# Kernel optimization log

Measured on AMD Instinct MI355X. Metric: run time of the kernel, lower is better.

The kernel has to match this reference:

```python
import jax, jax.numpy as jnp
import numpy as np

B, G = 32, 8          # batch, num_genres
N, T = 64, 64         # notes_size, timestep_size (input)
D, O = 32, 32         # notes_out, timestep_out (output)


def setup_inputs() -> dict:
    key = jax.random.key(0)
    k1, k2, k3, k4, k5 = jax.random.split(key, 5)
    x = jax.random.normal(k1, (B, N, T), dtype=jnp.float32)
    y = jax.random.uniform(k2, (B, G), dtype=jnp.float32)
    weight = jax.random.normal(k3, (G, D, O, N, T), dtype=jnp.float32) * 0.02
    bias = jax.random.normal(k4, (D * O,), dtype=jnp.float32) * 0.02
    mask = jax.random.randint(k5, (O, T), 0, 2).astype(jnp.float32)
    return {"x": x, "y": y, "weight": weight, "bias": bias, "mask": mask}


def reference(x, y, weight, bias, mask):
    # Fused form of:
    #   mw  = einsum('gdont,ot->gdont', weight, mask)
    #   mw2 = einsum('gdont,bg->bdont', mw, y)      # huge intermediate avoided
    #   out = einsum('bnt,bdont->bdo', x, mw2) + bias
    mw = weight * mask[None, None, :, None, :]          # (g,d,o,n,t)
    xw = jnp.einsum('bnt,gdont->bgdo', x, mw)           # contract n,t first
    out = jnp.einsum('bg,bgdo->bdo', y, xw)             # (b,d,o)
    return out + bias.reshape(D, O)[None, :, :]
```

## Files before the change

kernel.cpp:

```cpp
#include <hip/hip_runtime.h>
#include <hip/hip_bf16.h>

typedef __bf16 bf16x8 __attribute__((ext_vector_type(8)));
typedef float f32x4 __attribute__((ext_vector_type(4)));

#define G 8
#define B 32
#define D 32
#define O 32
#define K 4096
#define T 64
#define KSPLIT 2
#define KCHUNK (K / KSPLIT)
#define BK 256
#define NSTEP (KCHUNK / BK)
#define MROWS 16

#define XB_ELEMS (B * K)

__global__ __launch_bounds__(256) void prep_and_init(const float* __restrict__ x,
                                                     const float* __restrict__ bias,
                                                     __bf16* __restrict__ xb,
                                                     float* __restrict__ out) {
    int tid = blockIdx.x * 256 + threadIdx.x;
    if (tid < 16384) {
        int b = (tid >> 2) & 31;
        int k = (tid >> 7) * 32 + (tid & 3) * 8;
        const float4 x0 = *(const float4*)(x + b * K + k);
        const float4 x1 = *(const float4*)(x + b * K + k + 4);
        bf16x8 r;
        r[0] = (__bf16)x0.x; r[1] = (__bf16)x0.y; r[2] = (__bf16)x0.z; r[3] = (__bf16)x0.w;
        r[4] = (__bf16)x1.x; r[5] = (__bf16)x1.y; r[6] = (__bf16)x1.z; r[7] = (__bf16)x1.w;
        *(bf16x8*)(xb + (size_t)tid * 8) = r;
    } else {
        int t2 = tid - 16384;
        out[t2] = bias[t2 & 1023];
    }
}

__global__ __launch_bounds__(128) void gemm_main(const float* __restrict__ W,
                                                 const __bf16* __restrict__ xb,
                                                 const float* __restrict__ mask,
                                                 const float* __restrict__ y,
                                                 float* __restrict__ out) {
    __shared__ float ldsW[2][MROWS * BK];
    const int d = blockIdx.x, g = blockIdx.y;
    const int oh = blockIdx.z & 1, ks = blockIdx.z >> 1;
    const int wid  = threadIdx.x >> 6;
    const int lane = threadIdx.x & 63;
    const int bh = wid;
    const int l15 = lane & 15, g16 = lane >> 4;

    const int lds_ro = l15 * 1024 + ((g16 * 32) ^ ((l15 & 7) * 16));

    const float* mrow = mask + (oh * 16 + l15) * T + g16 * 8;
    const float4 me0 = *(const float4*)(mrow);
    const float4 me1 = *(const float4*)(mrow + 4);
    const float4 mo0 = *(const float4*)(mrow + 32);
    const float4 mo1 = *(const float4*)(mrow + 36);

    const __bf16* xbl = xb + (size_t)(ks * (KCHUNK / 32)) * 1024
                           + (bh * 16 + l15) * 32 + g16 * 8;

    const size_t wrow0 = ((size_t)(g * D + d) * O + oh * 16 + 8 * wid) * K
                         + (size_t)ks * KCHUNK;

    f32x4 acc = {0.f, 0.f, 0.f, 0.f};

#define STAGE(buf, step)                                                          \
    {                                                                             \
        _Pragma("unroll")                                                         \
        for (int i = 0; i < 8; ++i) {                                             \
            const int row = 8 * wid + i;                                          \
            const char* src = (const char*)(W + wrow0 + (size_t)i * K             \
                                            + (size_t)(step) * BK)                \
                              + ((lane * 16) ^ (i * 16));                         \
            __builtin_amdgcn_global_load_lds(                                     \
                (const __attribute__((address_space(1))) void*)src,               \
                (__attribute__((address_space(3))) void*)((char*)&ldsW[buf][0]    \
                                                          + row * 1024),          \
                16, 0,  2);                                             \
        }                                                                         \
    }

    STAGE(0, 0);
    __syncthreads();

    int cur = 0;
    for (int step = 0; step < NSTEP; ++step) {
        if (step + 1 < NSTEP) STAGE(cur ^ 1, step + 1);

        const char* lb = (const char*)&ldsW[cur][0];
        const __bf16* xs = xbl + (size_t)(step * 8) * 1024;
        #pragma unroll
        for (int s = 0; s < 8; ++s) {
            const int a0 = lds_ro + s * 128;
            const f32x4 alo = *(const f32x4*)(lb + a0);
            const f32x4 ahi = *(const f32x4*)(lb + (a0 ^ 16));
            const float4 ms0 = (s & 1) ? mo0 : me0;
            const float4 ms1 = (s & 1) ? mo1 : me1;
            bf16x8 af;
            af[0] = (__bf16)(alo[0] * ms0.x); af[1] = (__bf16)(alo[1] * ms0.y);
            af[2] = (__bf16)(alo[2] * ms0.z); af[3] = (__bf16)(alo[3] * ms0.w);
            af[4] = (__bf16)(ahi[0] * ms1.x); af[5] = (__bf16)(ahi[1] * ms1.y);
            af[6] = (__bf16)(ahi[2] * ms1.z); af[7] = (__bf16)(ahi[3] * ms1.w);
            const bf16x8 bfr = *(const bf16x8*)(xs + (size_t)s * 1024);
            acc = __builtin_amdgcn_mfma_f32_16x16x32_bf16(af, bfr, acc, 0, 0, 0);
        }
        __syncthreads();
        cur ^= 1;
    }
#undef STAGE

    const int bg = bh * 16 + l15;
    const float yv = y[bg * G + g];
    float* op = out + bg * (D * O) + d * O + oh * 16;
    #pragma unroll
    for (int i = 0; i < 4; ++i)
        unsafeAtomicAdd(op + g16 * 4 + i, yv * acc[i]);
}

extern "C" void kernel_launch(void* const* d_in, const int* in_sizes, int n_in,
                              void* d_out, int out_size, void* d_ws, size_t ws_size,
                              hipStream_t stream) {
    const float* x    = (const float*)d_in[0];
    const float* y    = (const float*)d_in[1];
    const float* w    = (const float*)d_in[2];
    const float* bias = (const float*)d_in[3];
    const float* mask = (const float*)d_in[4];
    float* out = (float*)d_out;

    __bf16* xbp = (__bf16*)d_ws;

    prep_and_init<<<192, 256, 0, stream>>>(x, bias, xbp, out);
    gemm_main<<<dim3(D, G, 4), 128, 0, stream>>>(w, xbp, mask, y, out);
}
```

Measured before the change: 37.60 us.

## Replace LDS-direct loads with register-staged triple-buffered prefetch pipeline

Weight tiles are now loaded with ordinary global loads into a three-deep register ring, prefetched three steps ahead, and written to double-buffered LDS after each compute step. The K loop is fully unrolled with scheduling barriers and explicit lgkmcnt waits plus raw s_barrier in place of __syncthreads. The goal is more memory-level parallelism, so the weight stream's global latency is hidden behind the MFMA work. The cost is higher register pressure from 24 f32x4 prefetch registers (launch bounds now request 2 blocks) and explicit LDS stores in place of direct-to-LDS loads.

```diff
diff --git a/kernel.cpp b/kernel.cpp
--- a/kernel.cpp
+++ b/kernel.cpp
@@ -38,11 +38,11 @@
     }
 }
 
-__global__ __launch_bounds__(128) void gemm_main(const float* __restrict__ W,
-                                                 const __bf16* __restrict__ xb,
-                                                 const float* __restrict__ mask,
-                                                 const float* __restrict__ y,
-                                                 float* __restrict__ out) {
+__global__ __launch_bounds__(128, 2) void gemm_main(const float* __restrict__ W,
+                                                    const __bf16* __restrict__ xb,
+                                                    const float* __restrict__ mask,
+                                                    const float* __restrict__ y,
+                                                    float* __restrict__ out) {
     __shared__ float ldsW[2][MROWS * BK];
     const int d = blockIdx.x, g = blockIdx.y;
     const int oh = blockIdx.z & 1, ks = blockIdx.z >> 1;
@@ -66,51 +66,76 @@
                          + (size_t)ks * KCHUNK;
 
     f32x4 acc = {0.f, 0.f, 0.f, 0.f};
+    f32x4 rg[3][8];
 
-#define STAGE(buf, step)                                                          \
+#define RELOAD(sA, stepn)                                                         \
+    {                                                                             \
+        _Pragma("unroll")                                                         \
+        for (int i = 0; i < 8; ++i)                                               \
+            rg[sA][i] = *(const f32x4*)(W + wrow0 + (size_t)i * K                 \
+                                        + (stepn) * BK + lane * 4);               \
+    }
+#define DSWRITE(buf, sB)                                                          \
     {                                                                             \
         _Pragma("unroll")                                                         \
         for (int i = 0; i < 8; ++i) {                                             \
             const int row = 8 * wid + i;                                          \
-            const char* src = (const char*)(W + wrow0 + (size_t)i * K             \
-                                            + (size_t)(step) * BK)                \
-                              + ((lane * 16) ^ (i * 16));                         \
-            __builtin_amdgcn_global_load_lds(                                     \
-                (const __attribute__((address_space(1))) void*)src,               \
-                (__attribute__((address_space(3))) void*)((char*)&ldsW[buf][0]    \
-                                                          + row * 1024),          \
-                16, 0,  2);                                             \
+            *(f32x4*)((char*)&ldsW[buf][0] + row * 1024                           \
+                      + ((lane * 16) ^ (i * 16))) = rg[sB][i];                    \
+        }                                                                         \
+    }
+#define COMPUTE(t)                                                                \
+    {                                                                             \
+        const char* lb = (const char*)&ldsW[(t) & 1][0];                          \
+        const __bf16* xs = xbl + (size_t)((t) * 8) * 1024;                        \
+        _Pragma("unroll")                                                         \
+        for (int s = 0; s < 8; ++s) {                                             \
+            const int a0 = lds_ro + s * 128;                                      \
+            const f32x4 alo = *(const f32x4*)(lb + a0);                           \
+            const f32x4 ahi = *(const f32x4*)(lb + (a0 ^ 16));                    \
+            const float4 ms0 = (s & 1) ? mo0 : me0;                               \
+            const float4 ms1 = (s & 1) ? mo1 : me1;                               \
+            bf16x8 af;                                                            \
+            af[0] = (__bf16)(alo[0] * ms0.x); af[1] = (__bf16)(alo[1] * ms0.y);   \
+            af[2] = (__bf16)(alo[2] * ms0.z); af[3] = (__bf16)(alo[3] * ms0.w);   \
+            af[4] = (__bf16)(ahi[0] * ms1.x); af[5] = (__bf16)(ahi[1] * ms1.y);   \
+            af[6] = (__bf16)(ahi[2] * ms1.z); af[7] = (__bf16)(ahi[3] * ms1.w);   \
+            const bf16x8 bfr = *(const bf16x8*)(xs + (size_t)s * 1024);           \
+            acc = __builtin_amdgcn_mfma_f32_16x16x32_bf16(af, bfr, acc, 0, 0, 0); \
+        }                                                                         \
+    }
+#define STEP(t, sA, sB)                                                           \
+    {                                                                             \
+        if ((t) + 3 < NSTEP) RELOAD(sA, (t) + 3);                                 \
+        __builtin_amdgcn_sched_barrier(0);                                        \
+        COMPUTE(t);                                                               \
+        __builtin_amdgcn_sched_barrier(0);                                        \
+        if ((t) + 1 < NSTEP) {                                                    \
+            DSWRITE(((t) + 1) & 1, sB);                                           \
+            asm volatile("s_waitcnt lgkmcnt(0)" ::: "memory");                    \
+            __builtin_amdgcn_s_barrier();                                         \
         }                                                                         \
     }
 
-    STAGE(0, 0);
-    __syncthreads();
+    RELOAD(0, 0);
+    RELOAD(1, 1);
+    RELOAD(2, 2);
+    DSWRITE(0, 0);
+    asm volatile("s_waitcnt lgkmcnt(0)" ::: "memory");
+    __builtin_amdgcn_s_barrier();
 
-    int cur = 0;
-    for (int step = 0; step < NSTEP; ++step) {
-        if (step + 1 < NSTEP) STAGE(cur ^ 1, step + 1);
-
-        const char* lb = (const char*)&ldsW[cur][0];
-        const __bf16* xs = xbl + (size_t)(step * 8) * 1024;
-        #pragma unroll
-        for (int s = 0; s < 8; ++s) {
-            const int a0 = lds_ro + s * 128;
-            const f32x4 alo = *(const f32x4*)(lb + a0);
-            const f32x4 ahi = *(const f32x4*)(lb + (a0 ^ 16));
-            const float4 ms0 = (s & 1) ? mo0 : me0;
-            const float4 ms1 = (s & 1) ? mo1 : me1;
-            bf16x8 af;
-            af[0] = (__bf16)(alo[0] * ms0.x); af[1] = (__bf16)(alo[1] * ms0.y);
-            af[2] = (__bf16)(alo[2] * ms0.z); af[3] = (__bf16)(alo[3] * ms0.w);
-            af[4] = (__bf16)(ahi[0] * ms1.x); af[5] = (__bf16)(ahi[1] * ms1.y);
-            af[6] = (__bf16)(ahi[2] * ms1.z); af[7] = (__bf16)(ahi[3] * ms1.w);
-            const bf16x8 bfr = *(const bf16x8*)(xs + (size_t)s * 1024);
-            acc = __builtin_amdgcn_mfma_f32_16x16x32_bf16(af, bfr, acc, 0, 0, 0);
-        }
-        __syncthreads();
-        cur ^= 1;
-    }
-#undef STAGE
+    STEP(0, 0, 1)
+    STEP(1, 1, 2)
+    STEP(2, 2, 0)
+    STEP(3, 0, 1)
+    STEP(4, 1, 2)
+    STEP(5, 2, 0)
+    STEP(6, 0, 1)
+    STEP(7, 1, 2)
+#undef RELOAD
+#undef DSWRITE
+#undef COMPUTE
+#undef STEP
 
     const int bg = bh * 16 + l15;
     const float yv = y[bg * G + g];
```

After: 43.73 us. +16.3%, slower.

## Replace LDS staging with direct register loads, single-wave blocks, deeper K-split

Applied to the files above, without the earlier changes.

Drops the LDS double-buffer built with global_load_lds and has each single-wave block load its weight rows straight into registers, using a three-deep software pipeline of loads ahead of the MFMAs. Each wave now covers both batch halves with two accumulators, so each masked weight fragment is converted once and feeds two MFMAs. K-split goes from 2 to 8, giving 4096 small blocks to raise memory-level parallelism on the weight stream. The cost is four times more atomic adds into the output and uncoalesced per-lane row reads of the weights.

```diff
diff --git a/kernel.cpp b/kernel.cpp
--- a/kernel.cpp
+++ b/kernel.cpp
@@ -10,11 +10,9 @@
 #define O 32
 #define K 4096
 #define T 64
-#define KSPLIT 2
-#define KCHUNK (K / KSPLIT)
-#define BK 256
-#define NSTEP (KCHUNK / BK)
-#define MROWS 16
+#define KSPLIT 8
+#define KCH (K / KSPLIT)
+#define NKT (KCH / 32)
 
 #define XB_ELEMS (B * K)
 
@@ -38,20 +36,15 @@
     }
 }
 
-__global__ __launch_bounds__(128) void gemm_main(const float* __restrict__ W,
-                                                 const __bf16* __restrict__ xb,
-                                                 const float* __restrict__ mask,
-                                                 const float* __restrict__ y,
-                                                 float* __restrict__ out) {
-    __shared__ float ldsW[2][MROWS * BK];
+__global__ __launch_bounds__(64, 4) void gemm_main(const float* __restrict__ W,
+                                                   const __bf16* __restrict__ xb,
+                                                   const float* __restrict__ mask,
+                                                   const float* __restrict__ y,
+                                                   float* __restrict__ out) {
     const int d = blockIdx.x, g = blockIdx.y;
     const int oh = blockIdx.z & 1, ks = blockIdx.z >> 1;
-    const int wid  = threadIdx.x >> 6;
-    const int lane = threadIdx.x & 63;
-    const int bh = wid;
+    const int lane = threadIdx.x;
     const int l15 = lane & 15, g16 = lane >> 4;
-
-    const int lds_ro = l15 * 1024 + ((g16 * 32) ^ ((l15 & 7) * 16));
 
     const float* mrow = mask + (oh * 16 + l15) * T + g16 * 8;
     const float4 me0 = *(const float4*)(mrow);
@@ -59,65 +52,67 @@
     const float4 mo0 = *(const float4*)(mrow + 32);
     const float4 mo1 = *(const float4*)(mrow + 36);
 
-    const __bf16* xbl = xb + (size_t)(ks * (KCHUNK / 32)) * 1024
-                           + (bh * 16 + l15) * 32 + g16 * 8;
+    const float* wl = W + ((size_t)(g * D + d) * O + oh * 16 + l15) * K
+                        + ks * KCH + g16 * 8;
+    const __bf16* xL = xb + (size_t)(ks * NKT) * 1024 + l15 * 32 + g16 * 8;
+    const __bf16* xH = xL + 512;
 
-    const size_t wrow0 = ((size_t)(g * D + d) * O + oh * 16 + 8 * wid) * K
-                         + (size_t)ks * KCHUNK;
+    f32x4 accL = {0.f, 0.f, 0.f, 0.f};
+    f32x4 accH = {0.f, 0.f, 0.f, 0.f};
 
-    f32x4 acc = {0.f, 0.f, 0.f, 0.f};
+    f32x4 w0_0, w1_0, w0_1, w1_1, w0_2, w1_2;
+    bf16x8 xl_0, xh_0, xl_1, xh_1, xl_2, xh_2;
 
-#define STAGE(buf, step)                                                          \
+#define LOADSET(p, ktl)                                                           \
     {                                                                             \
-        _Pragma("unroll")                                                         \
-        for (int i = 0; i < 8; ++i) {                                             \
-            const int row = 8 * wid + i;                                          \
-            const char* src = (const char*)(W + wrow0 + (size_t)i * K             \
-                                            + (size_t)(step) * BK)                \
-                              + ((lane * 16) ^ (i * 16));                         \
-            __builtin_amdgcn_global_load_lds(                                     \
-                (const __attribute__((address_space(1))) void*)src,               \
-                (__attribute__((address_space(3))) void*)((char*)&ldsW[buf][0]    \
-                                                          + row * 1024),          \
-                16, 0,  2);                                             \
-        }                                                                         \
+        w0_##p = *(const f32x4*)(wl + (ktl) * 32);                                \
+        w1_##p = *(const f32x4*)(wl + (ktl) * 32 + 4);                            \
+        xl_##p = *(const bf16x8*)(xL + (size_t)(ktl) * 1024);                     \
+        xh_##p = *(const bf16x8*)(xH + (size_t)(ktl) * 1024);                     \
+    }
+#define COMP(p, ktl)                                                              \
+    {                                                                             \
+        const float4 ms0 = ((ktl) & 1) ? mo0 : me0;                               \
+        const float4 ms1 = ((ktl) & 1) ? mo1 : me1;                               \
+        bf16x8 af;                                                                \
+        af[0] = (__bf16)(w0_##p[0] * ms0.x); af[1] = (__bf16)(w0_##p[1] * ms0.y); \
+        af[2] = (__bf16)(w0_##p[2] * ms0.z); af[3] = (__bf16)(w0_##p[3] * ms0.w); \
+        af[4] = (__bf16)(w1_##p[0] * ms1.x); af[5] = (__bf16)(w1_##p[1] * ms1.y); \
+        af[6] = (__bf16)(w1_##p[2] * ms1.z); af[7] = (__bf16)(w1_##p[3] * ms1.w); \
+        accL = __builtin_amdgcn_mfma_f32_16x16x32_bf16(af, xl_##p, accL, 0, 0, 0);\
+        accH = __builtin_amdgcn_mfma_f32_16x16x32_bf16(af, xh_##p, accH, 0, 0, 0);\
     }
 
-    STAGE(0, 0);
-    __syncthreads();
+    LOADSET(0, 0)
+    LOADSET(1, 1)
+    LOADSET(2, 2)  COMP(0, 0)
+    LOADSET(0, 3)  COMP(1, 1)
+    LOADSET(1, 4)  COMP(2, 2)
+    LOADSET(2, 5)  COMP(0, 3)
+    LOADSET(0, 6)  COMP(1, 4)
+    LOADSET(1, 7)  COMP(2, 5)
+    LOADSET(2, 8)  COMP(0, 6)
+    LOADSET(0, 9)  COMP(1, 7)
+    LOADSET(1, 10) COMP(2, 8)
+    LOADSET(2, 11) COMP(0, 9)
+    LOADSET(0, 12) COMP(1, 10)
+    LOADSET(1, 13) COMP(2, 11)
+    LOADSET(2, 14) COMP(0, 12)
+    LOADSET(0, 15) COMP(1, 13)
+    COMP(2, 14)
+    COMP(0, 15)
+#undef LOADSET
+#undef COMP
 
-    int cur = 0;
-    for (int step = 0; step < NSTEP; ++step) {
-        if (step + 1 < NSTEP) STAGE(cur ^ 1, step + 1);
-
-        const char* lb = (const char*)&ldsW[cur][0];
-        const __bf16* xs = xbl + (size_t)(step * 8) * 1024;
-        #pragma unroll
-        for (int s = 0; s < 8; ++s) {
-            const int a0 = lds_ro + s * 128;
-            const f32x4 alo = *(const f32x4*)(lb + a0);
-            const f32x4 ahi = *(const f32x4*)(lb + (a0 ^ 16));
-            const float4 ms0 = (s & 1) ? mo0 : me0;
-            const float4 ms1 = (s & 1) ? mo1 : me1;
-            bf16x8 af;
-            af[0] = (__bf16)(alo[0] * ms0.x); af[1] = (__bf16)(alo[1] * ms0.y);
-            af[2] = (__bf16)(alo[2] * ms0.z); af[3] = (__bf16)(alo[3] * ms0.w);
-            af[4] = (__bf16)(ahi[0] * ms1.x); af[5] = (__bf16)(ahi[1] * ms1.y);
-            af[6] = (__bf16)(ahi[2] * ms1.z); af[7] = (__bf16)(ahi[3] * ms1.w);
-            const bf16x8 bfr = *(const bf16x8*)(xs + (size_t)s * 1024);
-            acc = __builtin_amdgcn_mfma_f32_16x16x32_bf16(af, bfr, acc, 0, 0, 0);
-        }
-        __syncthreads();
-        cur ^= 1;
+    const float yv0 = y[l15 * G + g];
+    const float yv1 = y[(16 + l15) * G + g];
+    float* op0 = out + l15 * (D * O) + d * O + oh * 16 + g16 * 4;
+    float* op1 = op0 + 16 * (D * O);
+    #pragma unroll
+    for (int i = 0; i < 4; ++i) {
+        unsafeAtomicAdd(op0 + i, yv0 * accL[i]);
+        unsafeAtomicAdd(op1 + i, yv1 * accH[i]);
     }
-#undef STAGE
-
-    const int bg = bh * 16 + l15;
-    const float yv = y[bg * G + g];
-    float* op = out + bg * (D * O) + d * O + oh * 16;
-    #pragma unroll
-    for (int i = 0; i < 4; ++i)
-        unsafeAtomicAdd(op + g16 * 4 + i, yv * acc[i]);
 }
 
 extern "C" void kernel_launch(void* const* d_in, const int* in_sizes, int n_in,
@@ -133,5 +128,5 @@
     __bf16* xbp = (__bf16*)d_ws;
 
     prep_and_init<<<192, 256, 0, stream>>>(x, bias, xbp, out);
-    gemm_main<<<dim3(D, G, 4), 128, 0, stream>>>(w, xbp, mask, y, out);
+    gemm_main<<<dim3(D, G, 16), 64, 0, stream>>>(w, xbp, mask, y, out);
 }
```

Measured after the change: 59.75 us. 58.9% more time.
